# Optimization experiments

Hardware: AMD Instinct MI355X
Metric: run time of the kernel (lower is better)

Reference implementation:

```python
import jax, jax.numpy as jnp
import numpy as np

IMG_SIZE = 1280
NUM_ANCHORS = 3
NUM_CLASSES = 80
B, G = 16, 160
C = NUM_ANCHORS * (6 + NUM_CLASSES)  # 258


def setup_inputs() -> dict:
    key = jax.random.key(0)
    k1, k2, k3 = jax.random.split(key, 3)
    x = jax.random.normal(k1, (B, C, G, G), dtype=jnp.float32)
    target = jax.random.uniform(k2, (B, 50, 7), dtype=jnp.float32)
    # anchor box priors in pixels (positive sizes)
    anchors = jax.random.uniform(k3, (NUM_ANCHORS, 2), dtype=jnp.float32) * 60.0 + 4.0
    return {"x": x, "target": target, "anchors": anchors}


def reference(x, target, anchors):
    # x: [B, A*Cp, G, G] -> [B, A, G, G, Cp]
    Bb, Cc, Gg, _ = x.shape
    A = anchors.shape[0]
    Cp = Cc // A
    y = x.reshape(Bb, A, Cp, Gg, Gg).transpose(0, 1, 3, 4, 2)

    off_x = jax.nn.sigmoid(y[..., 0])          # [B,A,G,G]
    off_y = jax.nn.sigmoid(y[..., 1])
    scale_w = jnp.exp(y[..., 2])
    scale_h = jnp.exp(y[..., 3])
    anchor_yaw = y[..., 4]
    anchor_conf = jax.nn.sigmoid(y[..., 5])
    anchor_cls = jnp.argmax(y[..., 6:], axis=-1).astype(x.dtype)

    stride = IMG_SIZE / Gg
    grid = jnp.arange(Gg, dtype=x.dtype)
    grid_x = grid[None, :]   # broadcasts over rows (repeat((G,1)))
    grid_y = grid[:, None]   # its transpose

    anchor_x = jnp.floor((off_x + grid_x) * stride)
    anchor_y = jnp.floor((off_y + grid_y) * stride)
    anchor_w = scale_w * anchors[:, 0][None, :, None, None]
    anchor_h = scale_h * anchors[:, 1][None, :, None, None]

    # [B, A, G, G, 7] -> [B, A*G*G, 7]
    pred = jnp.stack(
        [anchor_x, anchor_y, anchor_w, anchor_h, anchor_yaw, anchor_conf, anchor_cls],
        axis=-1,
    ).reshape(Bb, A * Gg * Gg, 7)
    return pred
```

## Files before the change

### kernel.cpp

```cpp
#include <hip/hip_runtime.h>

namespace {

constexpr int Gg     = 160;
constexpr int NA     = 3;
constexpr int NB     = 16;
constexpr int CP     = 86;
constexpr int NCLS   = 80;
constexpr int PLANE  = Gg * Gg;
constexpr int QPP    = PLANE / 4;
constexpr int TOTAL  = NB * NA * QPP;
constexpr float STRIDE = 8.0f;
constexpr int LROW   = 29;

typedef float f4 __attribute__((ext_vector_type(4)));

union F4 { f4 v; float f[4]; };

__device__ __forceinline__ f4 ldnt(const float* p) {
    return __builtin_nontemporal_load(reinterpret_cast<const f4*>(p));
}

__device__ __forceinline__ float fsigmoid(float v) {
    return __builtin_amdgcn_rcpf(1.0f + __expf(-v));
}

__global__ __launch_bounds__(256, 6) void anchor_decode(
    const float* __restrict__ x,
    const float* __restrict__ anchors,
    float* __restrict__ out)
{
    __shared__ float lds[256 * LROW];

    const int t    = blockIdx.x * 256 + threadIdx.x;
    const int lane = threadIdx.x & 63;

    const int q   = t % QPP;
    const int ba  = t / QPP;
    const int a   = ba - (ba / NA) * NA;
    const int pix = q * 4;
    const int i   = pix / Gg;
    const int j   = pix - i * Gg;

    const float* xp = x + (size_t)ba * (CP * PLANE) + pix;
    const float* cp = xp + (size_t)6 * PLANE;

    float bval[4], bidx[4];
    #pragma unroll
    for (int p = 0; p < 4; ++p) { bval[p] = -__builtin_inff(); bidx[p] = 0.0f; }

    for (int c0 = 0; c0 < NCLS; c0 += 8) {
        F4 u[8];
        #pragma unroll
        for (int k = 0; k < 8; ++k)
            u[k].v = ldnt(cp + (size_t)(c0 + k) * PLANE);
        #pragma unroll
        for (int k = 0; k < 8; ++k) {
            const float fc = (float)(c0 + k);
            #pragma unroll
            for (int p = 0; p < 4; ++p) {
                const bool gt = u[k].f[p] > bval[p];
                bval[p] = gt ? u[k].f[p] : bval[p];
                bidx[p] = gt ? fc : bidx[p];
            }
        }
    }

    F4 h0, h1, h2, h3, h4, h5;
    h0.v = ldnt(xp + 0 * PLANE);
    h1.v = ldnt(xp + 1 * PLANE);
    h2.v = ldnt(xp + 2 * PLANE);
    h3.v = ldnt(xp + 3 * PLANE);
    h4.v = ldnt(xp + 4 * PLANE);
    h5.v = ldnt(xp + 5 * PLANE);

    const float aw = anchors[a * 2 + 0];
    const float ah = anchors[a * 2 + 1];
    const float fi = (float)i;
    const float fj = (float)j;

    float* lrow = lds + (size_t)threadIdx.x * LROW;
    #pragma unroll
    for (int p = 0; p < 4; ++p) {
        lrow[p * 7 + 0] = floorf((fsigmoid(h0.f[p]) + (fj + (float)p)) * STRIDE);
        lrow[p * 7 + 1] = floorf((fsigmoid(h1.f[p]) + fi) * STRIDE);
        lrow[p * 7 + 2] = __expf(h2.f[p]) * aw;
        lrow[p * 7 + 3] = __expf(h3.f[p]) * ah;
        lrow[p * 7 + 4] = h4.f[p];
        lrow[p * 7 + 5] = fsigmoid(h5.f[p]);
        lrow[p * 7 + 6] = bidx[p];
    }

    __syncthreads();

    const int wv = threadIdx.x >> 6;
    const float* wbase = lds + (size_t)wv * 64 * LROW;
    const int q0 = q - lane;
    float* op = out + ((size_t)ba * PLANE + (size_t)q0 * 4) * 7;

    #pragma unroll
    for (int k = 0; k < 7; ++k) {
        F4 w;
        #pragma unroll
        for (int e = 0; e < 4; ++e) {
            const int f = k * 256 + lane * 4 + e;
            w.f[e] = wbase[(f / 28) * LROW + (f % 28)];
        }
        __builtin_nontemporal_store(
            w.v, reinterpret_cast<f4*>(op + k * 256 + lane * 4));
    }
}

}

extern "C" void kernel_launch(void* const* d_in, const int* in_sizes, int n_in,
                              void* d_out, int out_size, void* d_ws, size_t ws_size,
                              hipStream_t stream) {
    const float* x       = (const float*)d_in[0];
    const float* anchors = (const float*)d_in[2];
    float* out           = (float*)d_out;

    const int blocks = (TOTAL + 255) / 256;
    anchor_decode<<<blocks, 256, 0, stream>>>(x, anchors, out);
}
```

Before: 528.1 us.

## Use single-wave blocks handling 16 pixels per thread with software-prefetched class loads

Each block shrinks from 256 threads to one 64-thread wavefront, and each thread processes four float4 groups (16 pixels) instead of four pixels. The class-argmax loop now double-buffers the next class plane's loads in registers. The aim is more memory-level parallelism per thread and a cheaper block-wide barrier, since the barrier now covers a single wave. The cost is higher register pressure and four times fewer threads in the grid, which may reduce occupancy and latency hiding.

```diff
diff --git a/kernel.cpp b/kernel.cpp
--- a/kernel.cpp
+++ b/kernel.cpp
@@ -8,8 +8,9 @@
 constexpr int CP     = 86;
 constexpr int NCLS   = 80;
 constexpr int PLANE  = Gg * Gg;
-constexpr int QPP    = PLANE / 4;
-constexpr int TOTAL  = NB * NA * QPP;
+constexpr int BPX    = 1024;
+constexpr int BLKPP  = PLANE / BPX;
+constexpr int NBLK   = NB * NA * BLKPP;
 constexpr float STRIDE = 8.0f;
 constexpr int LROW   = 29;
 
@@ -20,94 +21,104 @@
 __device__ __forceinline__ f4 ldnt(const float* p) {
     return __builtin_nontemporal_load(reinterpret_cast<const f4*>(p));
 }
-
+__device__ __forceinline__ void stnt(float* p, f4 v) {
+    __builtin_nontemporal_store(v, reinterpret_cast<f4*>(p));
+}
 __device__ __forceinline__ float fsigmoid(float v) {
     return __builtin_amdgcn_rcpf(1.0f + __expf(-v));
 }
 
-__global__ __launch_bounds__(256, 6) void anchor_decode(
+__global__ __launch_bounds__(64) void anchor_decode(
     const float* __restrict__ x,
     const float* __restrict__ anchors,
     float* __restrict__ out)
 {
     __shared__ float lds[256 * LROW];
 
-    const int t    = blockIdx.x * 256 + threadIdx.x;
-    const int lane = threadIdx.x & 63;
+    const int tid = threadIdx.x;
+    const int bid = blockIdx.x;
+    const int ba  = bid / BLKPP;
+    const int blk = bid - ba * BLKPP;
+    const int a   = ba % NA;
+    const int P0  = blk * BPX;
 
-    const int q   = t % QPP;
-    const int ba  = t / QPP;
-    const int a   = ba - (ba / NA) * NA;
-    const int pix = q * 4;
-    const int i   = pix / Gg;
-    const int j   = pix - i * Gg;
+    const float* base  = x + (size_t)ba * (CP * PLANE) + P0 + tid * 4;
+    const float* cbase = base + (size_t)6 * PLANE;
 
-    const float* xp = x + (size_t)ba * (CP * PLANE) + pix;
-    const float* cp = xp + (size_t)6 * PLANE;
+    float bval[4][4], bidx[4][4];
+    #pragma unroll
+    for (int k = 0; k < 4; ++k)
+        #pragma unroll
+        for (int p = 0; p < 4; ++p) { bval[k][p] = -__builtin_inff(); bidx[k][p] = 0.0f; }
 
-    float bval[4], bidx[4];
+    F4 cur[4], nxt[4];
     #pragma unroll
-    for (int p = 0; p < 4; ++p) { bval[p] = -__builtin_inff(); bidx[p] = 0.0f; }
+    for (int k = 0; k < 4; ++k) cur[k].v = ldnt(cbase + k * 256);
+    #pragma unroll
+    for (int k = 0; k < 4; ++k) nxt[k] = cur[k];
 
-    for (int c0 = 0; c0 < NCLS; c0 += 8) {
-        F4 u[8];
+    #pragma unroll 4
+    for (int c = 0; c < NCLS; ++c) {
+        if (c + 1 < NCLS) {
+            const float* np = cbase + (size_t)(c + 1) * PLANE;
+            #pragma unroll
+            for (int k = 0; k < 4; ++k) nxt[k].v = ldnt(np + k * 256);
+        }
+        const float fc = (float)c;
         #pragma unroll
-        for (int k = 0; k < 8; ++k)
-            u[k].v = ldnt(cp + (size_t)(c0 + k) * PLANE);
-        #pragma unroll
-        for (int k = 0; k < 8; ++k) {
-            const float fc = (float)(c0 + k);
+        for (int k = 0; k < 4; ++k)
             #pragma unroll
             for (int p = 0; p < 4; ++p) {
-                const bool gt = u[k].f[p] > bval[p];
-                bval[p] = gt ? u[k].f[p] : bval[p];
-                bidx[p] = gt ? fc : bidx[p];
+                const bool gt = cur[k].f[p] > bval[k][p];
+                bval[k][p] = gt ? cur[k].f[p] : bval[k][p];
+                bidx[k][p] = gt ? fc : bidx[k][p];
             }
-        }
+        #pragma unroll
+        for (int k = 0; k < 4; ++k) cur[k] = nxt[k];
     }
 
-    F4 h0, h1, h2, h3, h4, h5;
-    h0.v = ldnt(xp + 0 * PLANE);
-    h1.v = ldnt(xp + 1 * PLANE);
-    h2.v = ldnt(xp + 2 * PLANE);
-    h3.v = ldnt(xp + 3 * PLANE);
-    h4.v = ldnt(xp + 4 * PLANE);
-    h5.v = ldnt(xp + 5 * PLANE);
+    F4 h[6][4];
+    #pragma unroll
+    for (int c = 0; c < 6; ++c)
+        #pragma unroll
+        for (int k = 0; k < 4; ++k)
+            h[c][k].v = ldnt(base + (size_t)c * PLANE + k * 256);
 
     const float aw = anchors[a * 2 + 0];
     const float ah = anchors[a * 2 + 1];
-    const float fi = (float)i;
-    const float fj = (float)j;
 
-    float* lrow = lds + (size_t)threadIdx.x * LROW;
     #pragma unroll
-    for (int p = 0; p < 4; ++p) {
-        lrow[p * 7 + 0] = floorf((fsigmoid(h0.f[p]) + (fj + (float)p)) * STRIDE);
-        lrow[p * 7 + 1] = floorf((fsigmoid(h1.f[p]) + fi) * STRIDE);
-        lrow[p * 7 + 2] = __expf(h2.f[p]) * aw;
-        lrow[p * 7 + 3] = __expf(h3.f[p]) * ah;
-        lrow[p * 7 + 4] = h4.f[p];
-        lrow[p * 7 + 5] = fsigmoid(h5.f[p]);
-        lrow[p * 7 + 6] = bidx[p];
+    for (int k = 0; k < 4; ++k) {
+        const int pix = P0 + k * 256 + tid * 4;
+        const int i   = pix / Gg;
+        const int j   = pix - i * Gg;
+        const float fi = (float)i;
+        const float fj = (float)j;
+        float* lr = lds + (size_t)(k * 64 + tid) * LROW;
+        #pragma unroll
+        for (int p = 0; p < 4; ++p) {
+            lr[p * 7 + 0] = floorf((fsigmoid(h[0][k].f[p]) + (fj + (float)p)) * STRIDE);
+            lr[p * 7 + 1] = floorf((fsigmoid(h[1][k].f[p]) + fi) * STRIDE);
+            lr[p * 7 + 2] = __expf(h[2][k].f[p]) * aw;
+            lr[p * 7 + 3] = __expf(h[3][k].f[p]) * ah;
+            lr[p * 7 + 4] = h[4][k].f[p];
+            lr[p * 7 + 5] = fsigmoid(h[5][k].f[p]);
+            lr[p * 7 + 6] = bidx[k][p];
+        }
     }
 
     __syncthreads();
 
-    const int wv = threadIdx.x >> 6;
-    const float* wbase = lds + (size_t)wv * 64 * LROW;
-    const int q0 = q - lane;
-    float* op = out + ((size_t)ba * PLANE + (size_t)q0 * 4) * 7;
-
+    const size_t obase = ((size_t)ba * PLANE + P0) * 7;
     #pragma unroll
-    for (int k = 0; k < 7; ++k) {
+    for (int c = 0; c < 28; ++c) {
         F4 w;
         #pragma unroll
         for (int e = 0; e < 4; ++e) {
-            const int f = k * 256 + lane * 4 + e;
-            w.f[e] = wbase[(f / 28) * LROW + (f % 28)];
+            const int o = c * 256 + tid * 4 + e;
+            w.f[e] = lds[(o / 28) * LROW + (o % 28)];
         }
-        __builtin_nontemporal_store(
-            w.v, reinterpret_cast<f4*>(op + k * 256 + lane * 4));
+        stnt(out + obase + c * 256 + tid * 4, w.v);
     }
 }
 
@@ -120,6 +131,5 @@
     const float* anchors = (const float*)d_in[2];
     float* out           = (float*)d_out;
 
-    const int blocks = (TOTAL + 255) / 256;
-    anchor_decode<<<blocks, 256, 0, stream>>>(x, anchors, out);
+    anchor_decode<<<NBLK, 64, 0, stream>>>(x, anchors, out);
 }
```

After: 523.0 us. No clear change (-1.0%).
